# Performance work log

Measured on AMD Instinct MI355X. Metric: run time of the kernel, lower is better.

The kernel has to match this reference:

```python
import jax, jax.numpy as jnp
import numpy as np

V, SMAX, D, L, H, F = 50257, 1024, 768, 12, 12, 3072
DH = D // H
SCALE = float(np.sqrt(DH))


def setup_inputs() -> dict:
    key = jax.random.key(0)
    ks = jax.random.split(key, 24)
    B, S = 2, 1024
    std = 0.02
    inp = {
        'input_ids': jax.random.randint(ks[0], (B, S), 0, V),
        'tok_emb': jax.random.normal(ks[1], (V, D), jnp.float32) * std,
        'pos_emb': jax.random.normal(ks[2], (SMAX, D), jnp.float32) * std,
        # stacked per-layer params (leading dim L)
        'Wq': jax.random.normal(ks[3], (L, D, D), jnp.float32) * std,
        'bq': jnp.zeros((L, D), jnp.float32),
        'Wk': jax.random.normal(ks[4], (L, D, D), jnp.float32) * std,
        'bk': jnp.zeros((L, D), jnp.float32),
        'Wv': jax.random.normal(ks[5], (L, D, D), jnp.float32) * std,
        'bv': jnp.zeros((L, D), jnp.float32),
        'Wo': jax.random.normal(ks[6], (L, D, D), jnp.float32) * std,
        'bo': jnp.zeros((L, D), jnp.float32),
        'ln1_g': jnp.ones((L, D), jnp.float32),
        'ln1_b': jnp.zeros((L, D), jnp.float32),
        'ln2_g': jnp.ones((L, D), jnp.float32),
        'ln2_b': jnp.zeros((L, D), jnp.float32),
        'W1': jax.random.normal(ks[7], (L, D, F), jnp.float32) * std,
        'b1': jnp.zeros((L, F), jnp.float32),
        'W2': jax.random.normal(ks[8], (L, F, D), jnp.float32) * std,
        'b2': jnp.zeros((L, D), jnp.float32),
        'lnf_g': jnp.ones((D,), jnp.float32),
        'lnf_b': jnp.zeros((D,), jnp.float32),
        'Whead': jax.random.normal(ks[9], (D, V), jnp.float32) * std,
    }
    return inp


def _layernorm(x, g, b, eps=1e-5):
    mu = jnp.mean(x, axis=-1, keepdims=True)
    var = jnp.var(x, axis=-1, keepdims=True)
    return (x - mu) * jax.lax.rsqrt(var + eps) * g + b


def _gpt_forward(input_ids, tok_emb, pos_emb, Wq, bq, Wk, bk, Wv, bv, Wo, bo,
                 ln1_g, ln1_b, ln2_g, ln2_b, W1, b1, W2, b2, lnf_g, lnf_b, Whead):
    B, S = input_ids.shape
    x = tok_emb[input_ids] + pos_emb[:S][None, :, :]  # (B,S,D)
    # additive causal mask: -inf above the diagonal
    idx = jnp.arange(S)
    neg_inf = jnp.finfo(x.dtype).min
    mask = jnp.where(idx[None, :] > idx[:, None], neg_inf, 0.0).astype(x.dtype)  # (S,S)

    def block(x, p):
        (wq, bq_, wk, bk_, wv, bv_, wo, bo_, g1, b1_, g2, b2_, w1, bb1, w2, bb2) = p
        h = _layernorm(x, g1, b1_)
        q = (h @ wq + bq_).reshape(B, S, H, DH)
        k = (h @ wk + bk_).reshape(B, S, H, DH)
        v = (h @ wv + bv_).reshape(B, S, H, DH)
        scores = jnp.einsum('bqhd,bkhd->bhqk', q, k) / SCALE + mask
        attn = jax.nn.softmax(scores, axis=-1)
        o = jnp.einsum('bhqk,bkhd->bqhd', attn, v).reshape(B, S, D)
        x = x + (o @ wo + bo_)
        h2 = _layernorm(x, g2, b2_)
        ffn = jax.nn.gelu(h2 @ w1 + bb1, approximate=False) @ w2 + bb2
        return x + ffn, None

    params = (Wq, bq, Wk, bk, Wv, bv, Wo, bo, ln1_g, ln1_b, ln2_g, ln2_b, W1, b1, W2, b2)
    x, _ = jax.lax.scan(block, x, params)
    x = _layernorm(x, lnf_g, lnf_b)
    return x @ Whead  # (B,S,V) logits


def reference(input_ids, tok_emb, pos_emb, Wq, bq, Wk, bk, Wv, bv, Wo, bo,
              ln1_g, ln1_b, ln2_g, ln2_b, W1, b1, W2, b2, lnf_g, lnf_b, Whead):
    return _gpt_forward(input_ids, tok_emb, pos_emb, Wq, bq, Wk, bk, Wv, bv, Wo, bo,
                        ln1_g, ln1_b, ln2_g, ln2_b, W1, b1, W2, b2, lnf_g, lnf_b, Whead)
```

## Files before the change

### kernel.cpp

```cpp
#include <hip/hip_runtime.h>
#include <hip/hip_bf16.h>
#include <cstdint>
#include <cstddef>

#define DEV __device__ __forceinline__

typedef __attribute__((ext_vector_type(8))) short short8;
typedef __attribute__((ext_vector_type(4))) float f32x4;
typedef unsigned short u16;
typedef unsigned int u32;

static constexpr int Vv = 50257;
static constexpr int Dd = 768;
static constexpr int Ll = 12;
static constexpr int Hh = 12;
static constexpr int Ff = 3072;
static constexpr int Ss = 1024;
static constexpr int Bbatch = 2;
static constexpr int DHh = 64;
static constexpr int Mtok = Bbatch * Ss;
static constexpr int NQKV = 3 * Dd;
static constexpr int VPAD = 50304;

DEV float bf2f(u16 u){ u32 x = ((u32)u) << 16; float f; __builtin_memcpy(&f, &x, 4); return f; }
DEV u16 f2bf(float f){ u32 x; __builtin_memcpy(&x, &f, 4); x += 0x7fffu + ((x >> 16) & 1u); return (u16)(x >> 16); }

DEV void gld_lds16(const void* g, void* l){
  __builtin_amdgcn_global_load_lds((const __attribute__((address_space(1))) void*)g,
                                   (__attribute__((address_space(3))) void*)l, 16, 0, 0);
}

__global__ void k_embed(const int* __restrict__ ids, const float* __restrict__ tok,
                        const float* __restrict__ pos, float* __restrict__ x){
  int t = blockIdx.x;
  int id = ids[t];
  int s = t & (Ss - 1);
  const float* tr = tok + (size_t)id * Dd;
  const float* pr = pos + (size_t)s * Dd;
  float* xr = x + (size_t)t * Dd;
  for (int c = threadIdx.x; c < Dd; c += blockDim.x) xr[c] = tr[c] + pr[c];
}

__global__ __launch_bounds__(256) void k_ln(const float* __restrict__ x, const float* __restrict__ g,
                                            const float* __restrict__ b, u16* __restrict__ y){
  int row = blockIdx.x, tid = threadIdx.x;
  const float* xr = x + (size_t)row * Dd;
  float v0 = xr[tid], v1 = xr[tid + 256], v2 = xr[tid + 512];
  float s = v0 + v1 + v2, ss = v0 * v0 + v1 * v1 + v2 * v2;
  for (int o = 1; o < 64; o <<= 1){ s += __shfl_xor(s, o, 64); ss += __shfl_xor(ss, o, 64); }
  __shared__ float red[8];
  int w = tid >> 6, l = tid & 63;
  if (l == 0){ red[w] = s; red[w + 4] = ss; }
  __syncthreads();
  s = red[0] + red[1] + red[2] + red[3];
  ss = red[4] + red[5] + red[6] + red[7];
  float mu = s * (1.0f / Dd);
  float var = ss * (1.0f / Dd) - mu * mu;
  float rs = rsqrtf(var + 1e-5f);
  u16* yr = y + (size_t)row * Dd;
  yr[tid]       = f2bf((v0 - mu) * rs * g[tid]       + b[tid]);
  yr[tid + 256] = f2bf((v1 - mu) * rs * g[tid + 256] + b[tid + 256]);
  yr[tid + 512] = f2bf((v2 - mu) * rs * g[tid + 512] + b[tid + 512]);
}

__global__ void k_transpose(const float* __restrict__ src, u16* __restrict__ dst,
                            int R, int C, long smat, long dmat){
  __shared__ float tile[32][33];
  src += (size_t)blockIdx.z * smat;
  dst += (size_t)blockIdx.z * dmat;
  int c0 = blockIdx.x * 32, r0 = blockIdx.y * 32;
  int tx = threadIdx.x, ty = threadIdx.y;
  #pragma unroll
  for (int i = 0; i < 4; i++){
    int r = r0 + ty + i * 8, c = c0 + tx;
    if (c < C) tile[ty + i * 8][tx] = src[(size_t)r * C + c];
  }
  __syncthreads();
  #pragma unroll
  for (int i = 0; i < 4; i++){
    int c = c0 + ty + i * 8, r = r0 + tx;
    if (c < C) dst[(size_t)c * R + r] = f2bf(tile[tx][ty + i * 8]);
  }
}

__global__ void k_vt(const u16* __restrict__ qkv, u16* __restrict__ vt){
  __shared__ u16 tile[32][33];
  int z = blockIdx.z, b = z / Hh, h = z % Hh;
  int d0 = blockIdx.x * 32, s0 = blockIdx.y * 32;
  int tx = threadIdx.x, ty = threadIdx.y;
  #pragma unroll
  for (int i = 0; i < 4; i++){
    int sP = s0 + ty + i * 8;
    tile[ty + i * 8][tx] = qkv[(size_t)(b * Ss + sP) * NQKV + 2 * Dd + h * DHh + d0 + tx];
  }
  __syncthreads();
  #pragma unroll
  for (int i = 0; i < 4; i++){
    int d = d0 + ty + i * 8;
    vt[((size_t)(z * DHh + d)) * Ss + s0 + tx] = tile[tx][ty + i * 8];
  }
}

__global__ void k_biaspack(const float* __restrict__ bq, const float* __restrict__ bk,
                           const float* __restrict__ bv, float* __restrict__ o){
  int i = blockIdx.x * 256 + threadIdx.x;
  int col = i % NQKV, lay = i / NQKV;
  float v = (col < Dd) ? bq[lay * Dd + col]
          : (col < 2 * Dd) ? bk[lay * Dd + col - Dd]
          : bv[lay * Dd + col - 2 * Dd];
  o[i] = v;
}

__global__ __launch_bounds__(256) void k_combine(const float* __restrict__ p,
                                                 const float* __restrict__ bias,
                                                 float* __restrict__ x){
  int i = blockIdx.x * 256 + threadIdx.x;
  f32x4 a  = ((const f32x4*)x)[i];
  f32x4 q0 = ((const f32x4*)p)[i];
  f32x4 q1 = ((const f32x4*)(p + (size_t)Mtok * Dd))[i];
  int col0 = (i * 4) % Dd;
  f32x4 bv = *(const f32x4*)(bias + col0);
  ((f32x4*)x)[i] = a + q0 + q1 + bv;
}

template<int BM, int BN, int ACT, bool RES, bool OUTBF, bool SCALEQ, bool NB, bool HASBIAS, bool SPLIT>
__global__ __launch_bounds__(256) void k_gemm(const u16* __restrict__ A, const u16* __restrict__ Bt,
                                              const float* __restrict__ bias, const float* __restrict__ res,
                                              float* __restrict__ Cf, u16* __restrict__ Cb,
                                              int Mm, int Nn, int Kk, int MT, int NT, int KS){
  constexpr int HM = BM / 2, HN = BN / 2;
  constexpr int FM = HM / 16, FN = HN / 16;
  __shared__ __align__(16) u16 ldsA[2][BM * 32];
  __shared__ __align__(16) u16 ldsB[2][BN * 32];
  int tid = threadIdx.x, wid = tid >> 6, l = tid & 63;
  int wm = wid >> 1, wn = wid & 1;
  int lr = l & 15, lc = l >> 4;
  int nwg = gridDim.x, dIdx = blockIdx.x;
  int L = ((nwg & 7) == 0) ? ((dIdx & 7) * (nwg >> 3) + (dIdx >> 3)) : dIdx;
  int kidx = 0;
  if (SPLIT){ int per = MT * NT; kidx = L / per; L -= kidx * per; }
  int mtile = L % MT, ntile = L / MT;
  int m0 = mtile * BM, n0 = ntile * BN;
  int klen = Kk / KS, kbase = kidx * klen, nk = klen >> 5;

  f32x4 acc[FM][FN];
  #pragma unroll
  for (int i = 0; i < FM; i++)
    #pragma unroll
    for (int j = 0; j < FN; j++) acc[i][j] = (f32x4)0.0f;

  constexpr int nA = (BM * 4) / 256, nB = (BN * 4) / 256;
  auto stage = [&](int buf, int kk){
    #pragma unroll
    for (int i = 0; i < nA; i++){
      int id = i * 256 + tid, row = id >> 2, c = id & 3;
      int cs = c ^ ((row >> 1) & 3);
      gld_lds16(A + (size_t)(m0 + row) * Kk + kk + cs * 8,
                (char*)ldsA[buf] + (size_t)(i * 256 + (wid << 6)) * 16);
    }
    #pragma unroll
    for (int i = 0; i < nB; i++){
      int id = i * 256 + tid, row = id >> 2, c = id & 3;
      int cs = c ^ ((row >> 1) & 3);
      gld_lds16(Bt + (size_t)(n0 + row) * Kk + kk + cs * 8,
                (char*)ldsB[buf] + (size_t)(i * 256 + (wid << 6)) * 16);
    }
  };
  auto compute = [&](int buf){
    short8 af[FM], bfr[FN];
    #pragma unroll
    for (int i = 0; i < FM; i++){
      int row = wm * HM + i * 16 + lr;
      af[i] = *(const short8*)((const char*)ldsA[buf] + row * 64 + ((lc ^ ((row >> 1) & 3)) << 4));
    }
    #pragma unroll
    for (int j = 0; j < FN; j++){
      int row = wn * HN + j * 16 + lr;
      bfr[j] = *(const short8*)((const char*)ldsB[buf] + row * 64 + ((lc ^ ((row >> 1) & 3)) << 4));
    }
    #pragma unroll
    for (int i = 0; i < FM; i++)
      #pragma unroll
      for (int j = 0; j < FN; j++)
        acc[i][j] = __builtin_amdgcn_mfma_f32_16x16x32_bf16(af[i], bfr[j], acc[i][j], 0, 0, 0);
  };

  stage(0, kbase);
  __syncthreads();
  for (int t = 0; t < nk - 1; ++t){
    stage((t + 1) & 1, kbase + (t + 1) * 32);
    compute(t & 1);
    __syncthreads();
  }
  compute((nk - 1) & 1);

  if (SPLIT){
    float* P = Cf + (size_t)kidx * Mm * Nn;
    #pragma unroll
    for (int i = 0; i < FM; i++)
      #pragma unroll
      for (int j = 0; j < FN; j++){
        int col = n0 + wn * HN + j * 16 + lr;
        #pragma unroll
        for (int r = 0; r < 4; r++){
          int row = m0 + wm * HM + i * 16 + lc * 4 + r;
          P[(size_t)row * Nn + col] = acc[i][j][r];
        }
      }
    return;
  }
  #pragma unroll
  for (int i = 0; i < FM; i++){
    #pragma unroll
    for (int j = 0; j < FN; j++){
      int col = n0 + wn * HN + j * 16 + lr;
      if (NB && col >= Nn) continue;
      float bv = HASBIAS ? bias[col] : 0.0f;
      #pragma unroll
      for (int r = 0; r < 4; r++){
        int row = m0 + wm * HM + i * 16 + lc * 4 + r;
        float v = acc[i][j][r] + bv;
        if (SCALEQ){ if (col < Dd) v *= 0.125f; }
        if (ACT == 1) v = 0.5f * v * (1.0f + erff(v * 0.70710678118f));
        if (RES) v += res[(size_t)row * Nn + col];
        if (OUTBF) Cb[(size_t)row * Nn + col] = f2bf(v);
        else       Cf[(size_t)row * Nn + col] = v;
      }
    }
  }
}

__global__ __launch_bounds__(256) void k_attn(const u16* __restrict__ qkv, const u16* __restrict__ vt,
                                              u16* __restrict__ o){
  __shared__ __align__(16) u16 ldsK[64 * 64];
  __shared__ __align__(16) u16 ldsV[64 * 64];
  __shared__ __align__(16) u16 ldsP[4 * 16 * 72];
  int iq = blockIdx.x, bh = blockIdx.y, b = bh / Hh, h = bh % Hh;
  int tid = threadIdx.x, wid = tid >> 6, l = tid & 63, lr = l & 15, lc = l >> 4;
  int qrow = b * Ss + iq * 64 + wid * 16 + lr;
  const u16* qp = qkv + (size_t)qrow * NQKV + h * DHh;
  short8 qf[2];
  qf[0] = *(const short8*)(qp + lc * 8);
  qf[1] = *(const short8*)(qp + 32 + lc * 8);
  float mreg[4], lsum[4];
  f32x4 oacc[4];
  #pragma unroll
  for (int r = 0; r < 4; r++){ mreg[r] = -1e30f; lsum[r] = 0.0f; }
  #pragma unroll
  for (int i = 0; i < 4; i++) oacc[i] = (f32x4)0.0f;
  u16* pbase = ldsP + wid * 16 * 72;
  for (int j = 0; j <= iq; j++){
    #pragma unroll
    for (int c = 0; c < 2; c++){
      int id = c * 256 + tid, row = id >> 3, ch = id & 7;
      int cs = ch ^ (row & 7);
      gld_lds16(qkv + (size_t)(b * Ss + j * 64 + row) * NQKV + Dd + h * DHh + cs * 8,
                (char*)ldsK + (size_t)(c * 256 + (wid << 6)) * 16);
      gld_lds16(vt + ((size_t)(bh * DHh + row)) * Ss + j * 64 + cs * 8,
                (char*)ldsV + (size_t)(c * 256 + (wid << 6)) * 16);
    }
    __syncthreads();
    f32x4 sc[4];
    #pragma unroll
    for (int fn = 0; fn < 4; fn++) sc[fn] = (f32x4)0.0f;
    #pragma unroll
    for (int fn = 0; fn < 4; fn++){
      int kv = fn * 16 + lr;
      #pragma unroll
      for (int ks = 0; ks < 2; ks++){
        int ch = ks * 4 + lc;
        short8 kf = *(const short8*)((const char*)ldsK + kv * 128 + ((ch ^ (kv & 7)) << 4));
        sc[fn] = __builtin_amdgcn_mfma_f32_16x16x32_bf16(qf[ks], kf, sc[fn], 0, 0, 0);
      }
    }
    if (j == iq){
      #pragma unroll
      for (int fn = 0; fn < 4; fn++){
        int kv = fn * 16 + lr;
        #pragma unroll
        for (int r = 0; r < 4; r++){
          int qr = wid * 16 + lc * 4 + r;
          if (kv > qr) sc[fn][r] = -1e30f;
        }
      }
    }
    float alpha[4];
    #pragma unroll
    for (int r = 0; r < 4; r++){
      float mx = fmaxf(fmaxf(sc[0][r], sc[1][r]), fmaxf(sc[2][r], sc[3][r]));
      mx = fmaxf(mx, __shfl_xor(mx, 1, 64));
      mx = fmaxf(mx, __shfl_xor(mx, 2, 64));
      mx = fmaxf(mx, __shfl_xor(mx, 4, 64));
      mx = fmaxf(mx, __shfl_xor(mx, 8, 64));
      float mnew = fmaxf(mreg[r], mx);
      alpha[r] = __expf(mreg[r] - mnew);
      mreg[r] = mnew;
      float rsum = 0.0f;
      #pragma unroll
      for (int fn = 0; fn < 4; fn++){
        float p = __expf(sc[fn][r] - mnew);
        sc[fn][r] = p;
        rsum += p;
      }
      rsum += __shfl_xor(rsum, 1, 64);
      rsum += __shfl_xor(rsum, 2, 64);
      rsum += __shfl_xor(rsum, 4, 64);
      rsum += __shfl_xor(rsum, 8, 64);
      lsum[r] = lsum[r] * alpha[r] + rsum;
    }
    #pragma unroll
    for (int fn = 0; fn < 4; fn++)
      #pragma unroll
      for (int r = 0; r < 4; r++)
        pbase[(lc * 4 + r) * 72 + fn * 16 + lr] = f2bf(sc[fn][r]);
    #pragma unroll
    for (int fd = 0; fd < 4; fd++)
      #pragma unroll
      for (int r = 0; r < 4; r++) oacc[fd][r] *= alpha[r];
    short8 pa[2];
    #pragma unroll
    for (int ks = 0; ks < 2; ks++)
      pa[ks] = *(const short8*)((const char*)pbase + lr * 144 + (ks * 4 + lc) * 16);
    #pragma unroll
    for (int fd = 0; fd < 4; fd++){
      int dd = fd * 16 + lr;
      #pragma unroll
      for (int ks = 0; ks < 2; ks++){
        int ch = ks * 4 + lc;
        short8 vf = *(const short8*)((const char*)ldsV + dd * 128 + ((ch ^ (dd & 7)) << 4));
        oacc[fd] = __builtin_amdgcn_mfma_f32_16x16x32_bf16(pa[ks], vf, oacc[fd], 0, 0, 0);
      }
    }
    __syncthreads();
  }
  #pragma unroll
  for (int fd = 0; fd < 4; fd++)
    #pragma unroll
    for (int r = 0; r < 4; r++){
      int row = b * Ss + iq * 64 + wid * 16 + lc * 4 + r;
      o[(size_t)row * Dd + h * DHh + fd * 16 + lr] = f2bf(oacc[fd][r] / lsum[r]);
    }
}

extern "C" void kernel_launch(void* const* d_in, const int* in_sizes, int n_in,
                              void* d_out, int out_size, void* d_ws, size_t ws_size,
                              hipStream_t stream){
  const int*   ids  = (const int*)d_in[0];
  const float* tok  = (const float*)d_in[1];
  const float* pos  = (const float*)d_in[2];
  const float* Wq   = (const float*)d_in[3];
  const float* bq   = (const float*)d_in[4];
  const float* Wk   = (const float*)d_in[5];
  const float* bk   = (const float*)d_in[6];
  const float* Wv   = (const float*)d_in[7];
  const float* bv   = (const float*)d_in[8];
  const float* Wo   = (const float*)d_in[9];
  const float* bo   = (const float*)d_in[10];
  const float* ln1g = (const float*)d_in[11];
  const float* ln1b = (const float*)d_in[12];
  const float* ln2g = (const float*)d_in[13];
  const float* ln2b = (const float*)d_in[14];
  const float* W1   = (const float*)d_in[15];
  const float* b1   = (const float*)d_in[16];
  const float* W2   = (const float*)d_in[17];
  const float* b2   = (const float*)d_in[18];
  const float* lnfg = (const float*)d_in[19];
  const float* lnfb = (const float*)d_in[20];
  const float* Wh   = (const float*)d_in[21];
  float* out = (float*)d_out;

  auto al = [](size_t x){ return (x + 255) & ~(size_t)255; };
  size_t off = 0;
  auto take = [&](size_t bytes){ size_t r = off; off = al(off + bytes); return r; };
  size_t o_x    = take((size_t)Mtok * Dd * 4);
  size_t o_h    = take((size_t)Mtok * Dd * 2);
  size_t o_qkv  = take((size_t)Mtok * NQKV * 2);
  size_t o_vt   = take((size_t)Bbatch * Hh * DHh * Ss * 2);
  size_t o_o    = take((size_t)Mtok * Dd * 2);
  size_t o_mid  = take((size_t)Mtok * Ff * 2);
  size_t o_bq   = take((size_t)Ll * NQKV * 4);
  size_t o_part = take((size_t)2 * Mtok * Dd * 4);
  size_t o_rot = off;
  size_t o_wqkv, o_wo, o_w1, o_w2, o_wh;
  bool full;
  {
    size_t t = off;
    o_wqkv = t; t = al(t + (size_t)Ll * NQKV * Dd * 2);
    o_wo   = t; t = al(t + (size_t)Ll * Dd * Dd * 2);
    o_w1   = t; t = al(t + (size_t)Ll * Ff * Dd * 2);
    o_w2   = t; t = al(t + (size_t)Ll * Dd * Ff * 2);
    o_wh   = t; t = al(t + (size_t)VPAD * Dd * 2);
    full = (t <= ws_size);
  }
  char* ws = (char*)d_ws;
  float* x    = (float*)(ws + o_x);
  u16*   h    = (u16*)(ws + o_h);
  u16*   qkvb = (u16*)(ws + o_qkv);
  u16*   vtb  = (u16*)(ws + o_vt);
  u16*   ob   = (u16*)(ws + o_o);
  u16*   midb = (u16*)(ws + o_mid);
  float* bqkvp= (float*)(ws + o_bq);
  float* part = (float*)(ws + o_part);
  u16* wqkvT = full ? (u16*)(ws + o_wqkv) : (u16*)(ws + o_rot);
  u16* woT   = full ? (u16*)(ws + o_wo)   : (u16*)(ws + o_rot);
  u16* w1T   = full ? (u16*)(ws + o_w1)   : (u16*)(ws + o_rot);
  u16* w2T   = full ? (u16*)(ws + o_w2)   : (u16*)(ws + o_rot);
  u16* whT   = full ? (u16*)(ws + o_wh)   : (u16*)(ws + o_rot);

  dim3 tb(32, 8);
  auto tpose = [&](const float* src, u16* dst, int R, int C, int nmat, long smat, long dmat){
    k_transpose<<<dim3((C + 31) / 32, R / 32, nmat), tb, 0, stream>>>(src, dst, R, C, smat, dmat);
  };

  k_biaspack<<<(Ll * NQKV) / 256, 256, 0, stream>>>(bq, bk, bv, bqkvp);
  k_embed<<<Mtok, 256, 0, stream>>>(ids, tok, pos, x);

  if (full){
    tpose(Wq, wqkvT,              Dd, Dd, Ll, (long)Dd * Dd, (long)NQKV * Dd);
    tpose(Wk, wqkvT + Dd * Dd,    Dd, Dd, Ll, (long)Dd * Dd, (long)NQKV * Dd);
    tpose(Wv, wqkvT + 2 * Dd * Dd,Dd, Dd, Ll, (long)Dd * Dd, (long)NQKV * Dd);
    tpose(Wo, woT, Dd, Dd, Ll, (long)Dd * Dd, (long)Dd * Dd);
    tpose(W1, w1T, Dd, Ff, Ll, (long)Dd * Ff, (long)Ff * Dd);
    tpose(W2, w2T, Ff, Dd, Ll, (long)Ff * Dd, (long)Dd * Ff);
    tpose(Wh, whT, Dd, Vv, 1, 0, 0);
  }

  auto gemm_qkv = [&](const u16* A, const u16* Bt, const float* bias, u16* Cb){
    constexpr int MT = Mtok / 64, NT = NQKV / 128;
    k_gemm<64, 128, 0, false, true, true, false, true, false>
      <<<MT * NT, 256, 0, stream>>>(A, Bt, bias, nullptr, nullptr, Cb, Mtok, NQKV, Dd, MT, NT, 1);
  };
  auto gemm_wo = [&](const u16* A, const u16* Bt, const float* bias, float* C){
    constexpr int MT = Mtok / 64, NT = Dd / 64;
    k_gemm<64, 64, 0, true, false, false, false, true, false>
      <<<MT * NT, 256, 0, stream>>>(A, Bt, bias, C, C, nullptr, Mtok, Dd, Dd, MT, NT, 1);
  };
  auto gemm_ffn1 = [&](const u16* A, const u16* Bt, const float* bias, u16* Cb){
    constexpr int MT = Mtok / 64, NT = Ff / 128;
    k_gemm<64, 128, 1, false, true, false, false, true, false>
      <<<MT * NT, 256, 0, stream>>>(A, Bt, bias, nullptr, nullptr, Cb, Mtok, Ff, Dd, MT, NT, 1);
  };
  auto gemm_ffn2 = [&](const u16* A, const u16* Bt){
    constexpr int MT = Mtok / 64, NT = Dd / 64;
    k_gemm<64, 64, 0, false, false, false, false, false, true>
      <<<MT * NT * 2, 256, 0, stream>>>(A, Bt, nullptr, nullptr, part, nullptr, Mtok, Dd, Ff, MT, NT, 2);
  };
  auto gemm_head = [&](const u16* A, const u16* Bt, float* C){
    constexpr int MT = Mtok / 128, NT = VPAD / 128;
    k_gemm<128, 128, 0, false, false, false, true, false, false>
      <<<MT * NT, 256, 0, stream>>>(A, Bt, nullptr, nullptr, C, nullptr, Mtok, Vv, Dd, MT, NT, 1);
  };

  for (int l = 0; l < Ll; ++l){
    const u16* wqkvL = full ? wqkvT + (size_t)l * NQKV * Dd : wqkvT;
    const u16* woL   = full ? woT   + (size_t)l * Dd * Dd   : woT;
    const u16* w1L   = full ? w1T   + (size_t)l * Ff * Dd   : w1T;
    const u16* w2L   = full ? w2T   + (size_t)l * Dd * Ff   : w2T;
    if (!full){
      tpose(Wq + (size_t)l * Dd * Dd, wqkvT,              Dd, Dd, 1, 0, 0);
      tpose(Wk + (size_t)l * Dd * Dd, wqkvT + Dd * Dd,    Dd, Dd, 1, 0, 0);
      tpose(Wv + (size_t)l * Dd * Dd, wqkvT + 2 * Dd * Dd,Dd, Dd, 1, 0, 0);
    }
    k_ln<<<Mtok, 256, 0, stream>>>(x, ln1g + l * Dd, ln1b + l * Dd, h);
    gemm_qkv(h, wqkvL, bqkvp + l * NQKV, qkvb);
    k_vt<<<dim3(2, 32, Bbatch * Hh), tb, 0, stream>>>(qkvb, vtb);
    k_attn<<<dim3(Ss / 64, Bbatch * Hh), 256, 0, stream>>>(qkvb, vtb, ob);
    if (!full) tpose(Wo + (size_t)l * Dd * Dd, woT, Dd, Dd, 1, 0, 0);
    gemm_wo(ob, woL, bo + l * Dd, x);
    k_ln<<<Mtok, 256, 0, stream>>>(x, ln2g + l * Dd, ln2b + l * Dd, h);
    if (!full) tpose(W1 + (size_t)l * Dd * Ff, w1T, Dd, Ff, 1, 0, 0);
    gemm_ffn1(h, w1L, b1 + l * Ff, midb);
    if (!full) tpose(W2 + (size_t)l * Ff * Dd, w2T, Ff, Dd, 1, 0, 0);
    gemm_ffn2(midb, w2L);
    k_combine<<<(Mtok * Dd / 4) / 256, 256, 0, stream>>>(part, b2 + l * Dd, x);
  }
  k_ln<<<Mtok, 256, 0, stream>>>(x, lnfg, lnfb, h);
  if (!full) tpose(Wh, whT, Dd, Vv, 1, 0, 0);
  gemm_head(h, whT, out);
}
```

Baseline: 2.235 ms.

## Rework GEMM pipeline, fuse V-transpose into QKV epilogue, load attention K/V directly

The GEMM kernel is rewritten around compile-time K lengths, precomputed global and LDS pointers, explicit vmcnt waits with raw s_barriers, and setprio around the MFMA block, so the next tile's loads overlap compute with less address arithmetic. The QKV GEMM epilogue now also writes the transposed V, which removes the separate k_vt launch per layer. The attention kernel drops its shared-memory staging of K and V and per-tile __syncthreads, reading fragments straight from global memory. In exchange it relies on cache hits for those global reads, and the transposed-V scatter stores are uncoalesced.

```diff
diff --git a/kernel.cpp b/kernel.cpp
--- a/kernel.cpp
+++ b/kernel.cpp
@@ -22,12 +22,18 @@
 static constexpr int NQKV = 3 * Dd;
 static constexpr int VPAD = 50304;
 
-DEV float bf2f(u16 u){ u32 x = ((u32)u) << 16; float f; __builtin_memcpy(&f, &x, 4); return f; }
 DEV u16 f2bf(float f){ u32 x; __builtin_memcpy(&x, &f, 4); x += 0x7fffu + ((x >> 16) & 1u); return (u16)(x >> 16); }
 
 DEV void gld_lds16(const void* g, void* l){
   __builtin_amdgcn_global_load_lds((const __attribute__((address_space(1))) void*)g,
                                    (__attribute__((address_space(3))) void*)l, 16, 0, 0);
+}
+
+template<int N> DEV void waitv(){
+  if constexpr (N == 0) asm volatile("s_waitcnt vmcnt(0)" ::: "memory");
+  else if constexpr (N == 2) asm volatile("s_waitcnt vmcnt(2)" ::: "memory");
+  else if constexpr (N == 3) asm volatile("s_waitcnt vmcnt(3)" ::: "memory");
+  else if constexpr (N == 4) asm volatile("s_waitcnt vmcnt(4)" ::: "memory");
 }
 
 __global__ void k_embed(const int* __restrict__ ids, const float* __restrict__ tok,
@@ -83,24 +89,6 @@
   }
 }
 
-__global__ void k_vt(const u16* __restrict__ qkv, u16* __restrict__ vt){
-  __shared__ u16 tile[32][33];
-  int z = blockIdx.z, b = z / Hh, h = z % Hh;
-  int d0 = blockIdx.x * 32, s0 = blockIdx.y * 32;
-  int tx = threadIdx.x, ty = threadIdx.y;
-  #pragma unroll
-  for (int i = 0; i < 4; i++){
-    int sP = s0 + ty + i * 8;
-    tile[ty + i * 8][tx] = qkv[(size_t)(b * Ss + sP) * NQKV + 2 * Dd + h * DHh + d0 + tx];
-  }
-  __syncthreads();
-  #pragma unroll
-  for (int i = 0; i < 4; i++){
-    int d = d0 + ty + i * 8;
-    vt[((size_t)(z * DHh + d)) * Ss + s0 + tx] = tile[tx][ty + i * 8];
-  }
-}
-
 __global__ void k_biaspack(const float* __restrict__ bq, const float* __restrict__ bk,
                            const float* __restrict__ bv, float* __restrict__ o){
   int i = blockIdx.x * 256 + threadIdx.x;
@@ -123,25 +111,56 @@
   ((f32x4*)x)[i] = a + q0 + q1 + bv;
 }
 
-template<int BM, int BN, int ACT, bool RES, bool OUTBF, bool SCALEQ, bool NB, bool HASBIAS, bool SPLIT>
-__global__ __launch_bounds__(256) void k_gemm(const u16* __restrict__ A, const u16* __restrict__ Bt,
-                                              const float* __restrict__ bias, const float* __restrict__ res,
-                                              float* __restrict__ Cf, u16* __restrict__ Cb,
-                                              int Mm, int Nn, int Kk, int MT, int NT, int KS){
-  constexpr int HM = BM / 2, HN = BN / 2;
-  constexpr int FM = HM / 16, FN = HN / 16;
+template<int BM, int BN, int EPI>
+__global__ __launch_bounds__(256) void k_gemm2(const u16* __restrict__ A, const u16* __restrict__ Bt,
+    const float* __restrict__ bias, float* __restrict__ Cf, u16* __restrict__ Cb,
+    u16* __restrict__ vt, int Nn, int MT, int NT){
+  constexpr bool SPLIT = (EPI == 4);
+  constexpr int KST  = SPLIT ? Ff : Dd;
+  constexpr int KLEN = SPLIT ? (Ff / 2) : Dd;
+  constexpr int nk = KLEN / 32;
+  constexpr int HM = BM / 2, HN = BN / 2, FM = HM / 16, FN = HN / 16;
+  constexpr int nA = (BM * 4) / 256, nB = (BN * 4) / 256, NL = nA + nB;
   __shared__ __align__(16) u16 ldsA[2][BM * 32];
   __shared__ __align__(16) u16 ldsB[2][BN * 32];
   int tid = threadIdx.x, wid = tid >> 6, l = tid & 63;
   int wm = wid >> 1, wn = wid & 1;
   int lr = l & 15, lc = l >> 4;
   int nwg = gridDim.x, dIdx = blockIdx.x;
-  int L = ((nwg & 7) == 0) ? ((dIdx & 7) * (nwg >> 3) + (dIdx >> 3)) : dIdx;
+  int L = (dIdx & 7) * (nwg >> 3) + (dIdx >> 3);
   int kidx = 0;
   if (SPLIT){ int per = MT * NT; kidx = L / per; L -= kidx * per; }
   int mtile = L % MT, ntile = L / MT;
   int m0 = mtile * BM, n0 = ntile * BN;
-  int klen = Kk / KS, kbase = kidx * klen, nk = klen >> 5;
+  int kbase = kidx * KLEN;
+
+  const u16* gAp[nA]; const u16* gBp[nB];
+  u16 *dA0[nA], *dA1[nA], *dB0[nB], *dB1[nB];
+  #pragma unroll
+  for (int i = 0; i < nA; i++){
+    int id = i * 256 + tid, row = id >> 2, c = id & 3;
+    int cs = c ^ ((row >> 1) & 3);
+    gAp[i] = A + (size_t)(m0 + row) * KST + kbase + cs * 8;
+    dA0[i] = &ldsA[0][id * 8]; dA1[i] = &ldsA[1][id * 8];
+  }
+  #pragma unroll
+  for (int i = 0; i < nB; i++){
+    int id = i * 256 + tid, row = id >> 2, c = id & 3;
+    int cs = c ^ ((row >> 1) & 3);
+    gBp[i] = Bt + (size_t)(n0 + row) * KST + kbase + cs * 8;
+    dB0[i] = &ldsB[0][id * 8]; dB1[i] = &ldsB[1][id * 8];
+  }
+  int offA[FM], offB[FN];
+  #pragma unroll
+  for (int i = 0; i < FM; i++){
+    int row = wm * HM + i * 16 + lr;
+    offA[i] = row * 64 + ((lc ^ ((row >> 1) & 3)) << 4);
+  }
+  #pragma unroll
+  for (int j = 0; j < FN; j++){
+    int row = wn * HN + j * 16 + lr;
+    offB[j] = row * 64 + ((lc ^ ((row >> 1) & 3)) << 4);
+  }
 
   f32x4 acc[FM][FN];
   #pragma unroll
@@ -149,53 +168,53 @@
     #pragma unroll
     for (int j = 0; j < FN; j++) acc[i][j] = (f32x4)0.0f;
 
-  constexpr int nA = (BM * 4) / 256, nB = (BN * 4) / 256;
-  auto stage = [&](int buf, int kk){
-    #pragma unroll
-    for (int i = 0; i < nA; i++){
-      int id = i * 256 + tid, row = id >> 2, c = id & 3;
-      int cs = c ^ ((row >> 1) & 3);
-      gld_lds16(A + (size_t)(m0 + row) * Kk + kk + cs * 8,
-                (char*)ldsA[buf] + (size_t)(i * 256 + (wid << 6)) * 16);
-    }
-    #pragma unroll
-    for (int i = 0; i < nB; i++){
-      int id = i * 256 + tid, row = id >> 2, c = id & 3;
-      int cs = c ^ ((row >> 1) & 3);
-      gld_lds16(Bt + (size_t)(n0 + row) * Kk + kk + cs * 8,
-                (char*)ldsB[buf] + (size_t)(i * 256 + (wid << 6)) * 16);
-    }
-  };
-  auto compute = [&](int buf){
+  auto stage0 = [&]{
+    #pragma unroll
+    for (int i = 0; i < nA; i++){ gld_lds16(gAp[i], dA0[i]); gAp[i] += 32; }
+    #pragma unroll
+    for (int i = 0; i < nB; i++){ gld_lds16(gBp[i], dB0[i]); gBp[i] += 32; }
+  };
+  auto stage1 = [&]{
+    #pragma unroll
+    for (int i = 0; i < nA; i++){ gld_lds16(gAp[i], dA1[i]); gAp[i] += 32; }
+    #pragma unroll
+    for (int i = 0; i < nB; i++){ gld_lds16(gBp[i], dB1[i]); gBp[i] += 32; }
+  };
+  auto compute = [&](const u16* bA, const u16* bB){
     short8 af[FM], bfr[FN];
     #pragma unroll
-    for (int i = 0; i < FM; i++){
-      int row = wm * HM + i * 16 + lr;
-      af[i] = *(const short8*)((const char*)ldsA[buf] + row * 64 + ((lc ^ ((row >> 1) & 3)) << 4));
-    }
-    #pragma unroll
-    for (int j = 0; j < FN; j++){
-      int row = wn * HN + j * 16 + lr;
-      bfr[j] = *(const short8*)((const char*)ldsB[buf] + row * 64 + ((lc ^ ((row >> 1) & 3)) << 4));
-    }
+    for (int i = 0; i < FM; i++) af[i] = *(const short8*)((const char*)bA + offA[i]);
+    #pragma unroll
+    for (int j = 0; j < FN; j++) bfr[j] = *(const short8*)((const char*)bB + offB[j]);
+    __builtin_amdgcn_s_setprio(1);
     #pragma unroll
     for (int i = 0; i < FM; i++)
       #pragma unroll
       for (int j = 0; j < FN; j++)
         acc[i][j] = __builtin_amdgcn_mfma_f32_16x16x32_bf16(af[i], bfr[j], acc[i][j], 0, 0, 0);
-  };
-
-  stage(0, kbase);
-  __syncthreads();
-  for (int t = 0; t < nk - 1; ++t){
-    stage((t + 1) & 1, kbase + (t + 1) * 32);
-    compute(t & 1);
-    __syncthreads();
-  }
-  compute((nk - 1) & 1);
-
-  if (SPLIT){
-    float* P = Cf + (size_t)kidx * Mm * Nn;
+    __builtin_amdgcn_s_setprio(0);
+  };
+
+  stage0();
+  #pragma unroll 1
+  for (int t = 0; t < nk; t += 2){
+    __builtin_amdgcn_s_barrier();
+    __builtin_amdgcn_sched_barrier(0);
+    stage1(); waitv<NL>();
+    __builtin_amdgcn_s_barrier();
+    __builtin_amdgcn_sched_barrier(0);
+    compute(&ldsA[0][0], &ldsB[0][0]);
+    __builtin_amdgcn_s_barrier();
+    __builtin_amdgcn_sched_barrier(0);
+    if (t + 2 < nk){ stage0(); waitv<NL>(); }
+    else waitv<0>();
+    __builtin_amdgcn_s_barrier();
+    __builtin_amdgcn_sched_barrier(0);
+    compute(&ldsA[1][0], &ldsB[1][0]);
+  }
+
+  if (EPI == 4){
+    float* P = Cf + (size_t)kidx * Mtok * Dd;
     #pragma unroll
     for (int i = 0; i < FM; i++)
       #pragma unroll
@@ -204,7 +223,7 @@
         #pragma unroll
         for (int r = 0; r < 4; r++){
           int row = m0 + wm * HM + i * 16 + lc * 4 + r;
-          P[(size_t)row * Nn + col] = acc[i][j][r];
+          P[(size_t)row * Dd + col] = acc[i][j][r];
         }
       }
     return;
@@ -214,17 +233,27 @@
     #pragma unroll
     for (int j = 0; j < FN; j++){
       int col = n0 + wn * HN + j * 16 + lr;
-      if (NB && col >= Nn) continue;
-      float bv = HASBIAS ? bias[col] : 0.0f;
+      if (EPI == 0 && col >= Nn) continue;
+      float bv = (EPI == 1 || EPI == 2 || EPI == 3) ? bias[col] : 0.0f;
       #pragma unroll
       for (int r = 0; r < 4; r++){
         int row = m0 + wm * HM + i * 16 + lc * 4 + r;
         float v = acc[i][j][r] + bv;
-        if (SCALEQ){ if (col < Dd) v *= 0.125f; }
-        if (ACT == 1) v = 0.5f * v * (1.0f + erff(v * 0.70710678118f));
-        if (RES) v += res[(size_t)row * Nn + col];
-        if (OUTBF) Cb[(size_t)row * Nn + col] = f2bf(v);
-        else       Cf[(size_t)row * Nn + col] = v;
+        if (EPI == 1){ if (col < Dd) v *= 0.125f; }
+        if (EPI == 2) v = 0.5f * v * (1.0f + erff(v * 0.70710678118f));
+        if (EPI == 0){
+          Cf[(size_t)row * Nn + col] = v;
+        } else if (EPI == 3){
+          Cf[(size_t)row * Nn + col] += v;
+        } else {
+          u16 bvv = f2bf(v);
+          Cb[(size_t)row * Nn + col] = bvv;
+          if (EPI == 1 && col >= 2 * Dd){
+            int c2 = col - 2 * Dd, hh = c2 >> 6, dd2 = c2 & 63;
+            int bb = row >> 10, ss2 = row & 1023;
+            vt[((size_t)((bb * Hh + hh) * DHh + dd2) << 10) + ss2] = bvv;
+          }
+        }
       }
     }
   }
@@ -232,46 +261,38 @@
 
 __global__ __launch_bounds__(256) void k_attn(const u16* __restrict__ qkv, const u16* __restrict__ vt,
                                               u16* __restrict__ o){
-  __shared__ __align__(16) u16 ldsK[64 * 64];
-  __shared__ __align__(16) u16 ldsV[64 * 64];
-  __shared__ __align__(16) u16 ldsP[4 * 16 * 72];
+  __shared__ __align__(16) u16 ldsP[4][16 * 72];
   int iq = blockIdx.x, bh = blockIdx.y, b = bh / Hh, h = bh % Hh;
   int tid = threadIdx.x, wid = tid >> 6, l = tid & 63, lr = l & 15, lc = l >> 4;
   int qrow = b * Ss + iq * 64 + wid * 16 + lr;
   const u16* qp = qkv + (size_t)qrow * NQKV + h * DHh;
-  short8 qf[2];
-  qf[0] = *(const short8*)(qp + lc * 8);
-  qf[1] = *(const short8*)(qp + 32 + lc * 8);
+  short8 qf0 = *(const short8*)(qp + lc * 8);
+  short8 qf1 = *(const short8*)(qp + 32 + lc * 8);
+  const u16* kl = qkv + ((size_t)b * Ss) * NQKV + Dd + h * DHh + (size_t)lr * NQKV + lc * 8;
+  const u16* vl = vt + ((size_t)(bh * DHh) + lr) * Ss + lc * 8;
   float mreg[4], lsum[4];
   f32x4 oacc[4];
   #pragma unroll
   for (int r = 0; r < 4; r++){ mreg[r] = -1e30f; lsum[r] = 0.0f; }
   #pragma unroll
   for (int i = 0; i < 4; i++) oacc[i] = (f32x4)0.0f;
-  u16* pbase = ldsP + wid * 16 * 72;
-  for (int j = 0; j <= iq; j++){
-    #pragma unroll
-    for (int c = 0; c < 2; c++){
-      int id = c * 256 + tid, row = id >> 3, ch = id & 7;
-      int cs = ch ^ (row & 7);
-      gld_lds16(qkv + (size_t)(b * Ss + j * 64 + row) * NQKV + Dd + h * DHh + cs * 8,
-                (char*)ldsK + (size_t)(c * 256 + (wid << 6)) * 16);
-      gld_lds16(vt + ((size_t)(bh * DHh + row)) * Ss + j * 64 + cs * 8,
-                (char*)ldsV + (size_t)(c * 256 + (wid << 6)) * 16);
-    }
-    __syncthreads();
+  u16* pbase = ldsP[wid];
+  for (int j = 0; j <= iq; ++j){
+    const u16* kj = kl + (size_t)(j * 64) * NQKV;
+    const u16* vj = vl + j * 64;
+    short8 kf[4][2];
+    #pragma unroll
+    for (int fn = 0; fn < 4; fn++){
+      kf[fn][0] = *(const short8*)(kj + (size_t)(fn * 16) * NQKV);
+      kf[fn][1] = *(const short8*)(kj + (size_t)(fn * 16) * NQKV + 32);
+    }
     f32x4 sc[4];
     #pragma unroll
     for (int fn = 0; fn < 4; fn++) sc[fn] = (f32x4)0.0f;
     #pragma unroll
     for (int fn = 0; fn < 4; fn++){
-      int kv = fn * 16 + lr;
-      #pragma unroll
-      for (int ks = 0; ks < 2; ks++){
-        int ch = ks * 4 + lc;
-        short8 kf = *(const short8*)((const char*)ldsK + kv * 128 + ((ch ^ (kv & 7)) << 4));
-        sc[fn] = __builtin_amdgcn_mfma_f32_16x16x32_bf16(qf[ks], kf, sc[fn], 0, 0, 0);
-      }
+      sc[fn] = __builtin_amdgcn_mfma_f32_16x16x32_bf16(qf0, kf[fn][0], sc[fn], 0, 0, 0);
+      sc[fn] = __builtin_amdgcn_mfma_f32_16x16x32_bf16(qf1, kf[fn][1], sc[fn], 0, 0, 0);
     }
     if (j == iq){
       #pragma unroll
@@ -313,25 +334,21 @@
       #pragma unroll
       for (int r = 0; r < 4; r++)
         pbase[(lc * 4 + r) * 72 + fn * 16 + lr] = f2bf(sc[fn][r]);
+    asm volatile("s_waitcnt lgkmcnt(0)" ::: "memory");
+    __builtin_amdgcn_sched_barrier(0);
     #pragma unroll
     for (int fd = 0; fd < 4; fd++)
       #pragma unroll
       for (int r = 0; r < 4; r++) oacc[fd][r] *= alpha[r];
-    short8 pa[2];
-    #pragma unroll
-    for (int ks = 0; ks < 2; ks++)
-      pa[ks] = *(const short8*)((const char*)pbase + lr * 144 + (ks * 4 + lc) * 16);
+    short8 pa0 = *(const short8*)((const char*)pbase + lr * 144 + lc * 16);
+    short8 pa1 = *(const short8*)((const char*)pbase + lr * 144 + (4 + lc) * 16);
     #pragma unroll
     for (int fd = 0; fd < 4; fd++){
-      int dd = fd * 16 + lr;
-      #pragma unroll
-      for (int ks = 0; ks < 2; ks++){
-        int ch = ks * 4 + lc;
-        short8 vf = *(const short8*)((const char*)ldsV + dd * 128 + ((ch ^ (dd & 7)) << 4));
-        oacc[fd] = __builtin_amdgcn_mfma_f32_16x16x32_bf16(pa[ks], vf, oacc[fd], 0, 0, 0);
-      }
-    }
-    __syncthreads();
+      short8 vf0 = *(const short8*)(vj + (size_t)(fd * 16) * Ss);
+      short8 vf1 = *(const short8*)(vj + (size_t)(fd * 16) * Ss + 32);
+      oacc[fd] = __builtin_amdgcn_mfma_f32_16x16x32_bf16(pa0, vf0, oacc[fd], 0, 0, 0);
+      oacc[fd] = __builtin_amdgcn_mfma_f32_16x16x32_bf16(pa1, vf1, oacc[fd], 0, 0, 0);
+    }
   }
   #pragma unroll
   for (int fd = 0; fd < 4; fd++)
@@ -425,30 +442,25 @@
     tpose(Wh, whT, Dd, Vv, 1, 0, 0);
   }
 
-  auto gemm_qkv = [&](const u16* A, const u16* Bt, const float* bias, u16* Cb){
+  auto gemm_qkv = [&](const u16* Aop, const u16* Bop, const float* bias, u16* Cb){
     constexpr int MT = Mtok / 64, NT = NQKV / 128;
-    k_gemm<64, 128, 0, false, true, true, false, true, false>
-      <<<MT * NT, 256, 0, stream>>>(A, Bt, bias, nullptr, nullptr, Cb, Mtok, NQKV, Dd, MT, NT, 1);
-  };
-  auto gemm_wo = [&](const u16* A, const u16* Bt, const float* bias, float* C){
+    k_gemm2<64, 128, 1><<<MT * NT, 256, 0, stream>>>(Aop, Bop, bias, nullptr, Cb, vtb, NQKV, MT, NT);
+  };
+  auto gemm_wo = [&](const u16* Aop, const u16* Bop, const float* bias, float* C){
     constexpr int MT = Mtok / 64, NT = Dd / 64;
-    k_gemm<64, 64, 0, true, false, false, false, true, false>
-      <<<MT * NT, 256, 0, stream>>>(A, Bt, bias, C, C, nullptr, Mtok, Dd, Dd, MT, NT, 1);
-  };
-  auto gemm_ffn1 = [&](const u16* A, const u16* Bt, const float* bias, u16* Cb){
+    k_gemm2<64, 64, 3><<<MT * NT, 256, 0, stream>>>(Aop, Bop, bias, C, nullptr, nullptr, Dd, MT, NT);
+  };
+  auto gemm_ffn1 = [&](const u16* Aop, const u16* Bop, const float* bias, u16* Cb){
     constexpr int MT = Mtok / 64, NT = Ff / 128;
-    k_gemm<64, 128, 1, false, true, false, false, true, false>
-      <<<MT * NT, 256, 0, stream>>>(A, Bt, bias, nullptr, nullptr, Cb, Mtok, Ff, Dd, MT, NT, 1);
-  };
-  auto gemm_ffn2 = [&](const u16* A, const u16* Bt){
+    k_gemm2<64, 128, 2><<<MT * NT, 256, 0, stream>>>(Aop, Bop, bias, nullptr, Cb, nullptr, Ff, MT, NT);
+  };
+  auto gemm_ffn2 = [&](const u16* Aop, const u16* Bop){
     constexpr int MT = Mtok / 64, NT = Dd / 64;
-    k_gemm<64, 64, 0, false, false, false, false, false, true>
-      <<<MT * NT * 2, 256, 0, stream>>>(A, Bt, nullptr, nullptr, part, nullptr, Mtok, Dd, Ff, MT, NT, 2);
-  };
-  auto gemm_head = [&](const u16* A, const u16* Bt, float* C){
+    k_gemm2<64, 64, 4><<<MT * NT * 2, 256, 0, stream>>>(Aop, Bop, nullptr, part, nullptr, nullptr, Dd, MT, NT);
+  };
+  auto gemm_head = [&](const u16* Aop, const u16* Bop, float* C){
     constexpr int MT = Mtok / 128, NT = VPAD / 128;
-    k_gemm<128, 128, 0, false, false, false, true, false, false>
-      <<<MT * NT, 256, 0, stream>>>(A, Bt, nullptr, nullptr, C, nullptr, Mtok, Vv, Dd, MT, NT, 1);
+    k_gemm2<128, 128, 0><<<MT * NT, 256, 0, stream>>>(Aop, Bop, nullptr, C, nullptr, nullptr, Vv, MT, NT);
   };
 
   for (int l = 0; l < Ll; ++l){
@@ -463,7 +475,6 @@
     }
     k_ln<<<Mtok, 256, 0, stream>>>(x, ln1g + l * Dd, ln1b + l * Dd, h);
     gemm_qkv(h, wqkvL, bqkvp + l * NQKV, qkvb);
-    k_vt<<<dim3(2, 32, Bbatch * Hh), tb, 0, stream>>>(qkvb, vtb);
     k_attn<<<dim3(Ss / 64, Bbatch * Hh), 256, 0, stream>>>(qkvb, vtb, ob);
     if (!full) tpose(Wo + (size_t)l * Dd * Dd, woT, Dd, Dd, 1, 0, 0);
     gemm_wo(ob, woL, bo + l * Dd, x);
```

Result: slower. 2.618 ms (+17.2%).
